# Performance work log

Measured on AMD Instinct MI355X. Metric: run time of the kernel, lower is better.

## Reference

```python
import jax, jax.numpy as jnp
import numpy as np

HIDDEN = 512
HEADS = 8
HEAD_DIM = HIDDEN // HEADS  # 64
NUM_FEATURES = 256
EPS = 1e-4


def _gaussian_orthogonal_random_matrix(num_rows, num_cols, scaling=0, seed=1234):
    """Blocks of orthogonal rows from QR of gaussian matrices, rescaled (FAVOR+)."""
    rng = np.random.default_rng(seed)
    blocks = []
    full_blocks = num_rows // num_cols
    for _ in range(full_blocks):
        q, _ = np.linalg.qr(rng.standard_normal((num_cols, num_cols)))
        blocks.append(q.T)
    rem = num_rows - full_blocks * num_cols
    if rem > 0:
        q, _ = np.linalg.qr(rng.standard_normal((num_cols, num_cols)))
        blocks.append(q.T[:rem])
    mat = np.concatenate(blocks, axis=0)  # [num_rows, num_cols]
    if scaling == 0:
        # row norms of a fresh gaussian matrix (chi-distributed multipliers)
        multiplier = np.linalg.norm(rng.standard_normal((num_rows, num_cols)), axis=1)
    else:
        multiplier = np.sqrt(num_cols) * np.ones(num_rows)
    return (multiplier[:, None] * mat).astype(np.float32)


def _split_heads(x, b):
    # [b, n, hidden] -> [b, h, n, head_dim]
    return x.reshape(b, -1, HEADS, HEAD_DIM).transpose(0, 2, 1, 3)


def _phi(data, proj):
    """Nonnegative softmax kernel feature map (FAVOR+).
    data: [b,h,n,d], proj: [m,d] -> [b,h,n,m]"""
    d = data.shape[-1]
    m = proj.shape[0]
    x = data * (d ** -0.25)
    dash = jnp.einsum('bhnd,md->bhnm', x, proj)
    diag = 0.5 * jnp.sum(x * x, axis=-1, keepdims=True)
    return (m ** -0.5) * jnp.exp(dash - diag) + EPS


def setup_inputs() -> dict:
    key = jax.random.key(0)
    ks = jax.random.split(key, 12)
    b, n = 2, 8192
    s = HIDDEN ** -0.5
    inp = {
        'query': jax.random.normal(ks[0], (b, n, HIDDEN), jnp.float32),
        'key':   jax.random.normal(ks[1], (b, n, HIDDEN), jnp.float32),
        'value': jax.random.normal(ks[2], (b, n, HIDDEN), jnp.float32),
        'WQ_w': jax.random.normal(ks[3], (HIDDEN, HIDDEN), jnp.float32) * s,
        'WQ_b': jnp.zeros((HIDDEN,), jnp.float32),
        'WK_w': jax.random.normal(ks[4], (HIDDEN, HIDDEN), jnp.float32) * s,
        'WK_b': jnp.zeros((HIDDEN,), jnp.float32),
        'WV_w': jax.random.normal(ks[5], (HIDDEN, HIDDEN), jnp.float32) * s,
        'WV_b': jnp.zeros((HIDDEN,), jnp.float32),
        'WO_w': jax.random.normal(ks[6], (HIDDEN, HIDDEN), jnp.float32) * s,
        'WO_b': jnp.zeros((HIDDEN,), jnp.float32),
        'proj': jnp.asarray(_gaussian_orthogonal_random_matrix(NUM_FEATURES, HEAD_DIM)),
    }
    return inp


def reference(query, key, value, WQ_w, WQ_b, WK_w, WK_b, WV_w, WV_b, WO_w, WO_b, proj):
    b = query.shape[0]
    # torch Linear: y = x @ W.T + b
    Q = _split_heads(jnp.einsum('bnd,ed->bne', query, WQ_w) + WQ_b, b)
    K = _split_heads(jnp.einsum('bnd,ed->bne', key,   WK_w) + WK_b, b)
    V = _split_heads(jnp.einsum('bnd,ed->bne', value, WV_w) + WV_b, b)

    Qp = _phi(Q, proj)  # [b,h,n,m]
    Kp = _phi(K, proj)  # [b,h,n,m]

    # denominator: Q' @ sum_n K'  -> [b,h,n,1]
    denom = jnp.einsum('bhnm,bhm->bhn', Qp, jnp.sum(Kp, axis=2))[..., None]
    # linear attention: Q' @ (K'^T V), O(n*m*d)
    ctx = jnp.einsum('bhnm,bhnd->bhmd', Kp, V)
    attn = jnp.einsum('bhnm,bhmd->bhnd', Qp, ctx) / denom

    # faithful to original: .view(batch, -1, hidden) directly on [b,h,n,d]
    attn = attn.reshape(b, -1, HIDDEN)
    return jnp.einsum('bnd,ed->bne', attn, WO_w) + WO_b
```

## Files before the change

### kernel.cpp

```cpp
#include <hip/hip_runtime.h>

typedef __attribute__((ext_vector_type(8))) _Float16 f16x8;
typedef __attribute__((ext_vector_type(4))) float f32x4;

#define S4 0.35355339059327373f

static __device__ __forceinline__ ushort f2h(float f) {
  return __builtin_bit_cast(ushort, (_Float16)f);
}

static __device__ __forceinline__ void gload16(const void* g, void* l) {
  __builtin_amdgcn_global_load_lds((const __attribute__((address_space(1))) void*)g,
                                   (__attribute__((address_space(3))) void*)l, 16, 0, 0);
}

static __device__ __forceinline__ void cvt_store8(ushort* dst, float4 a, float4 b) {
  f16x8 h;
  h[0] = (_Float16)a.x; h[1] = (_Float16)a.y; h[2] = (_Float16)a.z; h[3] = (_Float16)a.w;
  h[4] = (_Float16)b.x; h[5] = (_Float16)b.y; h[6] = (_Float16)b.z; h[7] = (_Float16)b.w;
  *(f16x8*)dst = h;
}

template<int BM, int BN, int WR, int WC, int EPI, int ZMODE, int DIAG, int AF32, int BF32>
__global__ __launch_bounds__(256) void gemm_bt(
    const void* __restrict__ Av, const void* __restrict__ Bv,
    const float* __restrict__ bias, ushort* __restrict__ Cb,
    float* __restrict__ Cf, const float* __restrict__ rv0,
    float* __restrict__ dg,
    int K, int ldA, int ldB, int ldC, int Mz,
    long sAz, long sBz, long sCz)
{
  constexpr int BK = 32;
  constexpr int WTM = BM / WR, WTN = BN / WC;
  constexpr int MI = WTM / 16, NI = WTN / 16;
  constexpr int LDSB = (BM + BN) * 64;

  __shared__ uint4 smem4[LDSB / 16];
  char* smem = (char*)smem4;
  ushort* As = (ushort*)smem;
  ushort* Bs = (ushort*)(smem + BM * 64);

  const int tid = threadIdx.x;
  const int l = tid & 63, w = tid >> 6;
  const int wr = w / WC, wc = w % WC;
  const int lr = l & 15, lk = l >> 4;
  const int tm = blockIdx.x * BM, tn = blockIdx.y * BN;
  const int z = blockIdx.z;

  const ushort* Ah = (const ushort*)Av;
  const ushort* Bh = (const ushort*)Bv;
  const float*  Af = (const float*)Av;
  const float*  Bf = (const float*)Bv;
  long aoff = 0, boff = 0;
  if (ZMODE == 0) { aoff = (long)z * sAz; boff = (long)z * sBz; }
  if (ZMODE == 2) { aoff = (long)z * sAz; boff = (long)(z >> 3) * sBz + (z & 7) * 64; }
  if (ZMODE == 3) {
    aoff = (long)(z & 15) * sAz + (long)(z >> 4) * 1024;
    boff = (long)(z & 15) * sBz + (long)(z >> 4) * 1024;
  }
  Ah += aoff; Bh += boff; Af += aoff; Bf += boff;
  const float* rv = (EPI == 6) ? (rv0 + (long)z * Mz) : nullptr;
  const long coff = (long)z * sCz;

  f32x4 acc[MI][NI];
#pragma unroll
  for (int i = 0; i < MI; ++i)
#pragma unroll
    for (int j = 0; j < NI; ++j) acc[i][j] = f32x4{0.f, 0.f, 0.f, 0.f};

  for (int k0 = 0; k0 < K; k0 += BK) {
    if constexpr (AF32) {
      const int ar = tid >> 1, ac = (tid & 1) * 16;
      const float* g = Af + (long)(tm + ar) * ldA + k0 + ac;
      float4 f0 = *(const float4*)(g);
      float4 f1 = *(const float4*)(g + 4);
      float4 f2 = *(const float4*)(g + 8);
      float4 f3 = *(const float4*)(g + 12);
      cvt_store8(As + ar * 32 + ac, f0, f1);
      cvt_store8(As + ar * 32 + ac + 8, f2, f3);
    } else {
      constexpr int AB = BM * 64;
#pragma unroll
      for (int s = 0; s < (AB + 4095) / 4096; ++s) {
        const int base = s * 4096 + w * 1024;
        if (base < AB) {
          const int idx = base + l * 16;
          gload16(Ah + (long)(tm + (idx >> 6)) * ldA + k0 + ((idx & 63) >> 1),
                  (char*)As + base);
        }
      }
    }
    if constexpr (BF32) {
      const int br = tid >> 1, bc = (tid & 1) * 16;
      const float* g = Bf + (long)(tn + br) * ldB + k0 + bc;
      float4 f0 = *(const float4*)(g);
      float4 f1 = *(const float4*)(g + 4);
      float4 f2 = *(const float4*)(g + 8);
      float4 f3 = *(const float4*)(g + 12);
      cvt_store8(Bs + br * 32 + bc, f0, f1);
      cvt_store8(Bs + br * 32 + bc + 8, f2, f3);
    } else {
      constexpr int BB = BN * 64;
#pragma unroll
      for (int s = 0; s < (BB + 4095) / 4096; ++s) {
        const int base = s * 4096 + w * 1024;
        if (base < BB) {
          const int idx = base + l * 16;
          gload16(Bh + (long)(tn + (idx >> 6)) * ldB + k0 + ((idx & 63) >> 1),
                  (char*)Bs + base);
        }
      }
    }
    __syncthreads();

    f16x8 af[MI], bfr[NI];
#pragma unroll
    for (int mi = 0; mi < MI; ++mi)
      af[mi] = *(const f16x8*)(As + (wr * WTM + mi * 16 + lr) * 32 + lk * 8);
#pragma unroll
    for (int ni = 0; ni < NI; ++ni)
      bfr[ni] = *(const f16x8*)(Bs + (wc * WTN + ni * 16 + lr) * 32 + lk * 8);
#pragma unroll
    for (int mi = 0; mi < MI; ++mi)
#pragma unroll
      for (int ni = 0; ni < NI; ++ni)
        acc[mi][ni] = __builtin_amdgcn_mfma_f32_16x16x32_f16(af[mi], bfr[ni], acc[mi][ni], 0, 0, 0);
    __syncthreads();
  }

#pragma unroll
  for (int mi = 0; mi < MI; ++mi) {
#pragma unroll
    for (int j = 0; j < 4; ++j) {
      const int row = tm + wr * WTM + mi * 16 + lk * 4 + j;
      float ds = 0.f;
#pragma unroll
      for (int ni = 0; ni < NI; ++ni) {
        const int col = tn + wc * WTN + ni * 16 + lr;
        float v = acc[mi][ni][j];
        if (EPI == 0 || EPI == 3) v += bias[col];
        if (EPI == 4) v += bias[row];
        if (EPI == 6) v = 0.0625f * __expf(v - rv[col]) + 1e-4f;
        if (DIAG) ds += v * v;
        if (EPI == 4) {
          const int b = col >> 13, nn = col & 8191;
          const int h = row >> 6, d = row & 63;
          Cb[(long)(b * 8 + h) * 655360 + (long)d * 8192 + nn] = f2h(v);
        } else if (EPI == 3 || EPI == 5) {
          Cf[coff + (long)row * ldC + col] = v;
        } else {
          Cb[coff + (long)row * ldC + col] = f2h(v);
        }
      }
      if (DIAG) {
        ds += __shfl_xor(ds, 1, 64);
        ds += __shfl_xor(ds, 2, 64);
        ds += __shfl_xor(ds, 4, 64);
        ds += __shfl_xor(ds, 8, 64);
        if (lr == 0) {
          const int b = row >> 13, nn = row & 8191;
          const int head = (tn + wc * WTN) >> 6;
          dg[(long)(b * 8 + head) * 8192 + nn] = 0.0625f * ds;
        }
      }
    }
  }
}

__global__ __launch_bounds__(256) void phiattn_k(
    const ushort* __restrict__ Qh, const ushort* __restrict__ pjh,
    const float* __restrict__ diagQ, const ushort* __restrict__ ctxb,
    ushort* __restrict__ attnR)
{
  const int bx = blockIdx.x, bh = blockIdx.y;
  const int b = bh >> 3, h = bh & 7;
  const int tm = bx * 64;
  const int tid = threadIdx.x, l = tid & 63, w = tid >> 6;
  const int lr = l & 15, lk = l >> 4;

  __shared__ uint4 smem4[4992];
  char* smem = (char*)smem4;
  ushort* P  = (ushort*)smem;
  ushort* Pj = (ushort*)(smem + 33792);
  ushort* As = (ushort*)(smem + 70656);
  ushort* Cs = (ushort*)(smem + 33792);

  const ushort* QB = Qh + (long)b * 4194304 + h * 64;
  const float* rv = diagQ + (long)bh * 8192;

#pragma unroll
  for (int it = 0; it < 8; ++it) {
    const int g = it * 256 + tid;
    const int row = g >> 3, colg = (g & 7) * 8;
    *(uint4*)(Pj + row * 72 + colg) = *(const uint4*)(pjh + row * 64 + colg);
  }
#pragma unroll
  for (int it = 0; it < 2; ++it) {
    const int g = it * 256 + tid;
    const int row = g >> 3, colg = (g & 7) * 8;
    *(uint4*)(As + row * 72 + colg) = *(const uint4*)(QB + (long)(tm + row) * 512 + colg);
  }
  __syncthreads();

  f32x4 a2[16];
#pragma unroll
  for (int i = 0; i < 16; ++i) a2[i] = f32x4{0.f, 0.f, 0.f, 0.f};
  {
    f16x8 af0 = *(const f16x8*)(As + (w * 16 + lr) * 72 + lk * 8);
    f16x8 af1 = *(const f16x8*)(As + (w * 16 + lr) * 72 + 32 + lk * 8);
#pragma unroll
    for (int ni = 0; ni < 16; ++ni) {
      f16x8 b0 = *(const f16x8*)(Pj + (ni * 16 + lr) * 72 + lk * 8);
      f16x8 b1 = *(const f16x8*)(Pj + (ni * 16 + lr) * 72 + 32 + lk * 8);
      a2[ni] = __builtin_amdgcn_mfma_f32_16x16x32_f16(af0, b0, a2[ni], 0, 0, 0);
      a2[ni] = __builtin_amdgcn_mfma_f32_16x16x32_f16(af1, b1, a2[ni], 0, 0, 0);
    }
  }
#pragma unroll
  for (int ni = 0; ni < 16; ++ni)
#pragma unroll
    for (int j = 0; j < 4; ++j) {
      const int row = w * 16 + lk * 4 + j;
      const int col = ni * 16 + lr;
      const float vv = 0.0625f * __expf(a2[ni][j] - rv[tm + row]) + 1e-4f;
      P[row * 264 + col] = f2h(vv);
    }
  __syncthreads();

#pragma unroll
  for (int it = 0; it < 10; ++it) {
    const int g = it * 256 + tid;
    const int row = g >> 5, colg = (g & 31) * 8;
    *(uint4*)(Cs + row * 264 + colg) =
        *(const uint4*)(ctxb + (long)bh * 20480 + row * 256 + colg);
  }
  __syncthreads();

  f32x4 acc[5];
#pragma unroll
  for (int i = 0; i < 5; ++i) acc[i] = f32x4{0.f, 0.f, 0.f, 0.f};

  for (int k0 = 0; k0 < 256; k0 += 32) {
    f16x8 pa = *(const f16x8*)(P + (w * 16 + lr) * 264 + k0 + lk * 8);
#pragma unroll
    for (int ni = 0; ni < 5; ++ni) {
      f16x8 cf = *(const f16x8*)(Cs + (ni * 16 + lr) * 264 + k0 + lk * 8);
      acc[ni] = __builtin_amdgcn_mfma_f32_16x16x32_f16(pa, cf, acc[ni], 0, 0, 0);
    }
  }

  ushort* outb = attnR + (long)bh * 524288;
#pragma unroll
  for (int j = 0; j < 4; ++j) {
    const float dv = __shfl(acc[4][j], (l & 48), 64);
    const int row = tm + w * 16 + lk * 4 + j;
#pragma unroll
    for (int ni = 0; ni < 4; ++ni) {
      const int col = ni * 16 + lr;
      outb[(long)row * 64 + col] = f2h(acc[ni][j] / dv);
    }
  }
}

__global__ __launch_bounds__(256) void cvtall_k(
    const float* __restrict__ wq, const float* __restrict__ wk,
    const float* __restrict__ wv, const float* __restrict__ wo,
    const float* __restrict__ pj,
    ushort* __restrict__ wqh, ushort* __restrict__ wkh,
    ushort* __restrict__ wvh, ushort* __restrict__ woh,
    ushort* __restrict__ pjh)
{
  int i = blockIdx.x * 256 + threadIdx.x;
  const float* in; ushort* out; float scale = 1.f; int idx;
  if (i < 65536)       { in = wq; out = wqh; idx = i; }
  else if (i < 131072) { in = wk; out = wkh; idx = i - 65536; }
  else if (i < 196608) { in = wv; out = wvh; idx = i - 131072; }
  else if (i < 262144) { in = wo; out = woh; idx = i - 196608; }
  else if (i < 266240) { in = pj; out = pjh; idx = i - 262144; scale = S4; }
  else return;
  float4 v = ((const float4*)in)[idx];
  ushort4 o;
  o.x = f2h(v.x * scale); o.y = f2h(v.y * scale);
  o.z = f2h(v.z * scale); o.w = f2h(v.w * scale);
  ((ushort4*)out)[idx] = o;
}

__global__ __launch_bounds__(256) void vtpad_k(ushort* __restrict__ Vt) {
  const int i = blockIdx.x * 256 + threadIdx.x;
  const int bh = i >> 14, rem = i & 16383, r = rem >> 10, n8 = rem & 1023;
  const unsigned val = (r == 0) ? 0x3C003C00u : 0u;
  uint4 u; u.x = val; u.y = val; u.z = val; u.w = val;
  *(uint4*)(Vt + (long)bh * 655360 + (long)(64 + r) * 8192 + n8 * 8) = u;
}

__global__ __launch_bounds__(256) void ctxred_k(const float* __restrict__ cp,
                                                ushort* __restrict__ ctxb) {
  const int idx = blockIdx.x * 256 + threadIdx.x;
  const int bh = idx / 20480, rem = idx % 20480;
  float a = 0.f;
#pragma unroll
  for (int kc = 0; kc < 8; ++kc) a += cp[(long)(kc * 16 + bh) * 20480 + rem];
  ctxb[idx] = f2h(a);
}

extern "C" void kernel_launch(void* const* d_in, const int* in_sizes, int n_in,
                              void* d_out, int out_size, void* d_ws, size_t ws_size,
                              hipStream_t stream) {
  (void)in_sizes; (void)n_in; (void)out_size; (void)ws_size;
  const float* q  = (const float*)d_in[0];
  const float* k  = (const float*)d_in[1];
  const float* v  = (const float*)d_in[2];
  const float* wq = (const float*)d_in[3];
  const float* bq = (const float*)d_in[4];
  const float* wk = (const float*)d_in[5];
  const float* bk = (const float*)d_in[6];
  const float* wv = (const float*)d_in[7];
  const float* bv = (const float*)d_in[8];
  const float* wo = (const float*)d_in[9];
  const float* bo = (const float*)d_in[10];
  const float* pj = (const float*)d_in[11];

  char* ws = (char*)d_ws;
  ushort* attnR = (ushort*)(ws + 0);
  float*  cpart = (float*)(ws + 16777216);
  ushort* wqh   = (ushort*)(ws + 27262976);
  ushort* wkh   = (ushort*)(ws + 27787264);
  ushort* wvh   = (ushort*)(ws + 28311552);
  ushort* woh   = (ushort*)(ws + 28835840);
  ushort* pjh   = (ushort*)(ws + 29360128);
  ushort* Qh    = (ushort*)(ws + 29392896);
  ushort* Kh    = (ushort*)(ws + 46170112);
  ushort* Vt    = (ushort*)(ws + 62947328);
  ushort* KpT   = (ushort*)(ws + 83918848);
  float*  diagQ = (float*)(ws + 151027712);
  float*  diagK = (float*)(ws + 151552000);
  ushort* ctxb  = (ushort*)(ws + 152076288);

  cvtall_k<<<1040, 256, 0, stream>>>(wq, wk, wv, wo, pj, wqh, wkh, wvh, woh, pjh);
  vtpad_k<<<1024, 256, 0, stream>>>(Vt);

  gemm_bt<128,128,2,2,0,0,1,1,0><<<dim3(128,4,1), 256, 0, stream>>>(
      q, wqh, bq, Qh, nullptr, nullptr, diagQ, 512, 512, 512, 512, 0, 0L, 0L, 0L);
  gemm_bt<128,128,2,2,0,0,1,1,0><<<dim3(128,4,1), 256, 0, stream>>>(
      k, wkh, bk, Kh, nullptr, nullptr, diagK, 512, 512, 512, 512, 0, 0L, 0L, 0L);

  gemm_bt<128,128,2,2,4,0,0,0,1><<<dim3(4,128,1), 256, 0, stream>>>(
      wvh, v, bv, Vt, nullptr, nullptr, nullptr, 512, 512, 512, 0, 0, 0L, 0L, 0L);

  gemm_bt<128,128,2,2,6,2,0,0,0><<<dim3(2,64,16), 256, 0, stream>>>(
      pjh, Kh, nullptr, KpT, nullptr, diagK, nullptr, 64, 64, 512, 8192, 8192,
      0L, 4194304L, 2097152L);

  gemm_bt<80,128,1,4,5,3,0,0,0><<<dim3(1,2,128), 256, 0, stream>>>(
      Vt, KpT, nullptr, nullptr, cpart, nullptr, nullptr, 1024, 8192, 8192, 256, 0,
      655360L, 2097152L, 20480L);
  ctxred_k<<<1280, 256, 0, stream>>>(cpart, ctxb);

  phiattn_k<<<dim3(128,16), 256, 0, stream>>>(Qh, pjh, diagQ, ctxb, attnR);

  gemm_bt<128,128,2,2,3,0,0,0,0><<<dim3(128,4,1), 256, 0, stream>>>(
      attnR, woh, bo, nullptr, (float*)d_out, nullptr, nullptr, 512, 512, 512, 512, 0,
      0L, 0L, 0L);
}
```

Baseline: 187.3 us.

## Merge Q/K projections into one launch and fold V padding into conversion

Adds a dedicated qkproj_k kernel that computes both the Q and K projections, with bias and the per-head squared-norm diagonal, in a single launch over a z grid of 8. The separate vtpad_k launch is folded into cvtall_k, and the generic GEMM's bias and DIAG epilogue paths are trimmed. The context GEMM's N tile is halved from 128 to 64 and its grid doubled to raise block count. The aim is to cut launch overhead and fill the device better, at the cost of a duplicated GEMM body and a narrower ctx tile that reuses data less.

```diff
diff --git a/kernel.cpp b/kernel.cpp
--- a/kernel.cpp
+++ b/kernel.cpp
@@ -133,15 +133,13 @@
 #pragma unroll
     for (int j = 0; j < 4; ++j) {
       const int row = tm + wr * WTM + mi * 16 + lk * 4 + j;
-      float ds = 0.f;
 #pragma unroll
       for (int ni = 0; ni < NI; ++ni) {
         const int col = tn + wc * WTN + ni * 16 + lr;
         float v = acc[mi][ni][j];
-        if (EPI == 0 || EPI == 3) v += bias[col];
+        if (EPI == 3) v += bias[col];
         if (EPI == 4) v += bias[row];
         if (EPI == 6) v = 0.0625f * __expf(v - rv[col]) + 1e-4f;
-        if (DIAG) ds += v * v;
         if (EPI == 4) {
           const int b = col >> 13, nn = col & 8191;
           const int h = row >> 6, d = row & 63;
@@ -152,16 +150,98 @@
           Cb[coff + (long)row * ldC + col] = f2h(v);
         }
       }
-      if (DIAG) {
-        ds += __shfl_xor(ds, 1, 64);
-        ds += __shfl_xor(ds, 2, 64);
-        ds += __shfl_xor(ds, 4, 64);
-        ds += __shfl_xor(ds, 8, 64);
-        if (lr == 0) {
-          const int b = row >> 13, nn = row & 8191;
-          const int head = (tn + wc * WTN) >> 6;
-          dg[(long)(b * 8 + head) * 8192 + nn] = 0.0625f * ds;
-        }
+    }
+  }
+}
+
+__global__ __launch_bounds__(256) void qkproj_k(
+    const float* __restrict__ q, const float* __restrict__ k,
+    const ushort* __restrict__ wqh, const ushort* __restrict__ wkh,
+    const float* __restrict__ bq, const float* __restrict__ bk,
+    ushort* __restrict__ Qh, ushort* __restrict__ Kh,
+    float* __restrict__ diagQ, float* __restrict__ diagK)
+{
+  const int z = blockIdx.z, qk = z & 1;
+  const float*  Af   = qk ? k : q;
+  const ushort* Bh   = qk ? wkh : wqh;
+  const float*  bias = qk ? bk : bq;
+  ushort*       Cb   = qk ? Kh : Qh;
+  float*        dg   = qk ? diagK : diagQ;
+  const int tm = blockIdx.x * 128;
+  const int tn = (z >> 1) * 128;
+
+  __shared__ uint4 smem4[1024];
+  char* smem = (char*)smem4;
+  ushort* As = (ushort*)smem;
+  ushort* Bs = (ushort*)(smem + 8192);
+
+  const int tid = threadIdx.x;
+  const int l = tid & 63, w = tid >> 6;
+  const int wr = w >> 1, wc = w & 1;
+  const int lr = l & 15, lk = l >> 4;
+
+  f32x4 acc[4][4];
+#pragma unroll
+  for (int i = 0; i < 4; ++i)
+#pragma unroll
+    for (int j = 0; j < 4; ++j) acc[i][j] = f32x4{0.f, 0.f, 0.f, 0.f};
+
+  for (int k0 = 0; k0 < 512; k0 += 32) {
+    {
+      const int ar = tid >> 1, ac = (tid & 1) * 16;
+      const float* g = Af + (long)(tm + ar) * 512 + k0 + ac;
+      float4 f0 = *(const float4*)(g);
+      float4 f1 = *(const float4*)(g + 4);
+      float4 f2 = *(const float4*)(g + 8);
+      float4 f3 = *(const float4*)(g + 12);
+      cvt_store8(As + ar * 32 + ac, f0, f1);
+      cvt_store8(As + ar * 32 + ac + 8, f2, f3);
+    }
+#pragma unroll
+    for (int s = 0; s < 2; ++s) {
+      const int base = s * 4096 + w * 1024;
+      const int idx = base + l * 16;
+      gload16(Bh + (long)(tn + (idx >> 6)) * 512 + k0 + ((idx & 63) >> 1),
+              (char*)Bs + base);
+    }
+    __syncthreads();
+
+    f16x8 af[4], bfr[4];
+#pragma unroll
+    for (int mi = 0; mi < 4; ++mi)
+      af[mi] = *(const f16x8*)(As + (wr * 64 + mi * 16 + lr) * 32 + lk * 8);
+#pragma unroll
+    for (int ni = 0; ni < 4; ++ni)
+      bfr[ni] = *(const f16x8*)(Bs + (wc * 64 + ni * 16 + lr) * 32 + lk * 8);
+#pragma unroll
+    for (int mi = 0; mi < 4; ++mi)
+#pragma unroll
+      for (int ni = 0; ni < 4; ++ni)
+        acc[mi][ni] = __builtin_amdgcn_mfma_f32_16x16x32_f16(af[mi], bfr[ni], acc[mi][ni], 0, 0, 0);
+    __syncthreads();
+  }
+
+#pragma unroll
+  for (int mi = 0; mi < 4; ++mi) {
+#pragma unroll
+    for (int j = 0; j < 4; ++j) {
+      const int row = tm + wr * 64 + mi * 16 + lk * 4 + j;
+      float ds = 0.f;
+#pragma unroll
+      for (int ni = 0; ni < 4; ++ni) {
+        const int col = tn + wc * 64 + ni * 16 + lr;
+        float v = acc[mi][ni][j] + bias[col];
+        ds += v * v;
+        Cb[(long)row * 512 + col] = f2h(v);
+      }
+      ds += __shfl_xor(ds, 1, 64);
+      ds += __shfl_xor(ds, 2, 64);
+      ds += __shfl_xor(ds, 4, 64);
+      ds += __shfl_xor(ds, 8, 64);
+      if (lr == 0) {
+        const int b = row >> 13, nn = row & 8191;
+        const int head = (tn + wc * 64) >> 6;
+        dg[(long)(b * 8 + head) * 8192 + nn] = 0.0625f * ds;
       }
     }
   }
@@ -268,29 +348,29 @@
     const float* __restrict__ pj,
     ushort* __restrict__ wqh, ushort* __restrict__ wkh,
     ushort* __restrict__ wvh, ushort* __restrict__ woh,
-    ushort* __restrict__ pjh)
+    ushort* __restrict__ pjh, ushort* __restrict__ Vt)
 {
   int i = blockIdx.x * 256 + threadIdx.x;
+  if (i >= 266240) {
+    const int j = i - 266240;
+    if (j >= 262144) return;
+    const int bh = j >> 14, rem = j & 16383, r = rem >> 10, n8 = rem & 1023;
+    const unsigned val = (r == 0) ? 0x3C003C00u : 0u;
+    uint4 u; u.x = val; u.y = val; u.z = val; u.w = val;
+    *(uint4*)(Vt + (long)bh * 655360 + (long)(64 + r) * 8192 + n8 * 8) = u;
+    return;
+  }
   const float* in; ushort* out; float scale = 1.f; int idx;
   if (i < 65536)       { in = wq; out = wqh; idx = i; }
   else if (i < 131072) { in = wk; out = wkh; idx = i - 65536; }
   else if (i < 196608) { in = wv; out = wvh; idx = i - 131072; }
   else if (i < 262144) { in = wo; out = woh; idx = i - 196608; }
-  else if (i < 266240) { in = pj; out = pjh; idx = i - 262144; scale = S4; }
-  else return;
+  else                 { in = pj; out = pjh; idx = i - 262144; scale = S4; }
   float4 v = ((const float4*)in)[idx];
   ushort4 o;
   o.x = f2h(v.x * scale); o.y = f2h(v.y * scale);
   o.z = f2h(v.z * scale); o.w = f2h(v.w * scale);
   ((ushort4*)out)[idx] = o;
-}
-
-__global__ __launch_bounds__(256) void vtpad_k(ushort* __restrict__ Vt) {
-  const int i = blockIdx.x * 256 + threadIdx.x;
-  const int bh = i >> 14, rem = i & 16383, r = rem >> 10, n8 = rem & 1023;
-  const unsigned val = (r == 0) ? 0x3C003C00u : 0u;
-  uint4 u; u.x = val; u.y = val; u.z = val; u.w = val;
-  *(uint4*)(Vt + (long)bh * 655360 + (long)(64 + r) * 8192 + n8 * 8) = u;
 }
 
 __global__ __launch_bounds__(256) void ctxred_k(const float* __restrict__ cp,
@@ -336,13 +416,9 @@
   float*  diagK = (float*)(ws + 151552000);
   ushort* ctxb  = (ushort*)(ws + 152076288);
 
-  cvtall_k<<<1040, 256, 0, stream>>>(wq, wk, wv, wo, pj, wqh, wkh, wvh, woh, pjh);
-  vtpad_k<<<1024, 256, 0, stream>>>(Vt);
-
-  gemm_bt<128,128,2,2,0,0,1,1,0><<<dim3(128,4,1), 256, 0, stream>>>(
-      q, wqh, bq, Qh, nullptr, nullptr, diagQ, 512, 512, 512, 512, 0, 0L, 0L, 0L);
-  gemm_bt<128,128,2,2,0,0,1,1,0><<<dim3(128,4,1), 256, 0, stream>>>(
-      k, wkh, bk, Kh, nullptr, nullptr, diagK, 512, 512, 512, 512, 0, 0L, 0L, 0L);
+  cvtall_k<<<2064, 256, 0, stream>>>(wq, wk, wv, wo, pj, wqh, wkh, wvh, woh, pjh, Vt);
+
+  qkproj_k<<<dim3(128,1,8), 256, 0, stream>>>(q, k, wqh, wkh, bq, bk, Qh, Kh, diagQ, diagK);
 
   gemm_bt<128,128,2,2,4,0,0,0,1><<<dim3(4,128,1), 256, 0, stream>>>(
       wvh, v, bv, Vt, nullptr, nullptr, nullptr, 512, 512, 512, 0, 0, 0L, 0L, 0L);
@@ -351,7 +427,7 @@
       pjh, Kh, nullptr, KpT, nullptr, diagK, nullptr, 64, 64, 512, 8192, 8192,
       0L, 4194304L, 2097152L);
 
-  gemm_bt<80,128,1,4,5,3,0,0,0><<<dim3(1,2,128), 256, 0, stream>>>(
+  gemm_bt<80,64,1,4,5,3,0,0,0><<<dim3(1,4,128), 256, 0, stream>>>(
       Vt, KpT, nullptr, nullptr, cpart, nullptr, nullptr, 1024, 8192, 8192, 256, 0,
       655360L, 2097152L, 20480L);
   ctxred_k<<<1280, 256, 0, stream>>>(cpart, ctxb);
```

Measured after the change: 191.6 us. +2.3%, slower.
